# Kernel optimization log

Measured on AMD Instinct MI355X. Metric: run time of the kernel, lower is better.

## Reference

```python
import jax, jax.numpy as jnp
import numpy as np
import math

B, NOUT, NCLASSES, CENTER, TOPK = 1024, 512, 5994, 3, 5
M, SUB_M, SCALE = 0.2, -0.06, 30.0

COS_M, SIN_M = math.cos(M), math.sin(M)
TH, MM = math.cos(math.pi - M), math.sin(math.pi - M) * M
SUB_COS_M, SUB_SIN_M = math.cos(SUB_M), math.sin(SUB_M)
SUB_TH, SUB_MM = math.cos(math.pi - SUB_M), math.sin(math.pi - SUB_M) * SUB_M


def setup_inputs() -> dict:
    key = jax.random.key(0)
    k1, k2, k3 = jax.random.split(key, 3)
    x = jax.random.normal(k1, (B, NOUT), dtype=jnp.float32)
    # xavier_normal over (center, nClasses, nOut): fan_in=nClasses*nOut, fan_out=center*nOut
    std = math.sqrt(2.0 / (NCLASSES * NOUT + CENTER * NOUT))
    weight = jax.random.normal(k2, (CENTER, NCLASSES, NOUT), dtype=jnp.float32) * std
    label = jax.random.randint(k3, (B,), 0, NCLASSES, dtype=jnp.int64)
    return {"x": x, "weight": weight, "label": label}


def _l2norm(v, axis=-1, eps=1e-12):
    return v / jnp.maximum(jnp.linalg.norm(v, axis=axis, keepdims=True), eps)


def reference(x, weight, label):
    xn = _l2norm(x)                       # [B, j]
    wn = _l2norm(weight)                  # [a, c, j]
    cosine_subcen = jnp.einsum('bj,acj->bac', xn, wn)   # [B, center, C]
    cosine = jnp.max(cosine_subcen, axis=1)             # [B, C]

    sine = jnp.sqrt(jnp.clip(1.0 - cosine * cosine, 0.0, 1.0))
    phi = jnp.where(cosine - TH > 0, cosine * COS_M - sine * SIN_M, cosine - MM)
    sub_phi = jnp.where(cosine - SUB_TH > 0,
                        cosine * SUB_COS_M - sine * SUB_SIN_M,
                        cosine - SUB_MM)

    # topk+1 candidates; drop the label column if present, else drop the last
    _, idx = jax.lax.top_k(cosine, TOPK + 1)            # [B, topk+1]
    is_label = (idx == label[:, None].astype(idx.dtype))
    # stable sort pushes the (unique) label hit to the end, preserving order otherwise
    order = jnp.argsort(is_label.astype(jnp.int32), axis=1, stable=True)
    idx_fixed = jnp.take_along_axis(idx, order[:, :TOPK], axis=1)   # [B, topk]

    rows = jnp.arange(B)[:, None]
    one_hot_sub = jnp.zeros_like(cosine).at[rows, idx_fixed].add(1.0)
    one_hot = jax.nn.one_hot(label, NCLASSES, dtype=cosine.dtype)

    output = (one_hot * phi + one_hot_sub * sub_phi
              + (1.0 - one_hot_sub - one_hot) * cosine) * SCALE

    logp = jax.nn.log_softmax(output, axis=-1)
    loss = -jnp.mean(logp[jnp.arange(B), label])

    pred = jnp.argmax(cosine * SCALE, axis=-1)
    prec1 = jnp.mean((pred == label).astype(jnp.float32)) * 100.0
    return loss, prec1
```

## Files before the change

kernel.cpp:

```cpp
#include <hip/hip_runtime.h>
#include <math.h>

#define NB 1024
#define NC 5994
#define NCP 6144
#define NK 512
#define NA 3
#define NT 48
#define SCALE_F 30.0f
#define NPT 24

#define COS_M_F 0.9800665778412416f
#define SIN_M_F 0.19866933079506122f
#define TH_F (-0.9800665778412416f)
#define MM_F 0.039733866159012244f
#define SUB_COS_M_F 0.9982005399352042f
#define SUB_SIN_M_F (-0.05996400647944459f)
#define SUB_TH_F (-0.9982005399352042f)
#define SUB_MM_F 0.0035978403887666754f

typedef __attribute__((ext_vector_type(8))) short short8;
typedef __attribute__((ext_vector_type(4))) float f32x4;

__device__ __forceinline__ float waveReduceSum(float v) {
#pragma unroll
  for (int off = 32; off > 0; off >>= 1) v += __shfl_down(v, off);
  return v;
}

__device__ __forceinline__ void waveArgMax(float& v, int& i) {
#pragma unroll
  for (int off = 32; off > 0; off >>= 1) {
    float ov = __shfl_down(v, off);
    int oi = __shfl_down(i, off);
    if (ov > v || (ov == v && (unsigned)oi < (unsigned)i)) { v = ov; i = oi; }
  }
}

__device__ __forceinline__ ushort f2bf(float f) {
  unsigned u = __float_as_uint(f);
  u += 0x7FFFu + ((u >> 16) & 1u);
  return (ushort)(u >> 16);
}

__device__ __forceinline__ void load_lds16(const ushort* g, ushort* l) {
  __builtin_amdgcn_global_load_lds(
      (const __attribute__((address_space(1))) unsigned int*)g,
      (__attribute__((address_space(3))) unsigned int*)l, 16, 0, 0);
}

__global__ __launch_bounds__(256) void norm_convert(const float* __restrict__ x,
                                                    const float* __restrict__ w,
                                                    ushort* __restrict__ xb,
                                                    ushort* __restrict__ wb) {
  const int row = blockIdx.x * 4 + (threadIdx.x >> 6);
  const int lane = threadIdx.x & 63;
  const float* src;
  ushort* dst;
  if (row < NB) {
    src = x + (size_t)row * NK;
    dst = xb + (size_t)row * NK;
  } else {
    const int r = row - NB;
    const int a = r / NCP, c = r % NCP;
    dst = wb + (size_t)r * NK;
    if (c >= NC) {
      ushort4 z = {0, 0, 0, 0};
      *(ushort4*)(dst + lane * 4) = z;
      *(ushort4*)(dst + 256 + lane * 4) = z;
      return;
    }
    src = w + ((size_t)a * NC + c) * NK;
  }
  const float4 v0 = *(const float4*)(src + lane * 4);
  const float4 v1 = *(const float4*)(src + 256 + lane * 4);
  float ss = v0.x * v0.x + v0.y * v0.y + v0.z * v0.z + v0.w * v0.w +
             v1.x * v1.x + v1.y * v1.y + v1.z * v1.z + v1.w * v1.w;
  ss = waveReduceSum(ss);
  ss = __shfl(ss, 0);
  const float rn = 1.0f / fmaxf(sqrtf(ss), 1e-12f);
  ushort4 o0 = {f2bf(v0.x * rn), f2bf(v0.y * rn), f2bf(v0.z * rn), f2bf(v0.w * rn)};
  ushort4 o1 = {f2bf(v1.x * rn), f2bf(v1.y * rn), f2bf(v1.z * rn), f2bf(v1.w * rn)};
  *(ushort4*)(dst + lane * 4) = o0;
  *(ushort4*)(dst + 256 + lane * 4) = o1;
}

__global__ __launch_bounds__(128) void cos_gemm_mfma(const ushort* __restrict__ Xb,
                                                     const ushort* __restrict__ Wb,
                                                     float* __restrict__ cosine) {
  __shared__ ushort sA0[64 * 32];
  __shared__ ushort sA1[64 * 32];
  __shared__ ushort sB0[128 * 32];
  __shared__ ushort sB1[128 * 32];
  const int tid = threadIdx.x;
  const int lane = tid & 63;
  const int w = tid >> 6;

  const int id = blockIdx.x;
  const int cx = (id & 7) + ((id >> 7) << 3);
  const int by = (id >> 3) & 15;
  const int b0 = by * 64;
  const int c0 = cx * 128;

  const int lrow = lane >> 2;
  const int skg = ((lane & 3) - ((lane >> 3) & 3)) & 3;
  const ushort* gA = Xb + (size_t)(b0 + w * 32 + lrow) * NK + skg * 8;
  const ushort* gB = Wb + (size_t)(c0 + w * 64 + lrow) * NK + skg * 8;
  const int ldsA = w * 1024;
  const int ldsB = w * 2048;
  const int w4 = w * 4;

  const int r = lane & 15;
  const int kg = lane >> 4;
  const int rdoff = r * 32 + (((kg + (r >> 1)) & 3) * 8);

  f32x4 best[4][4];
  f32x4 acc[4][4];
#pragma unroll
  for (int i = 0; i < 4; ++i)
#pragma unroll
    for (int j = 0; j < 4; ++j) {
#pragma unroll
      for (int q = 0; q < 4; ++q) best[i][j][q] = -INFINITY;
      acc[i][j] = (f32x4)(0.f);
    }

  load_lds16(gA, (ushort*)sA0 + ldsA);
  load_lds16(gA + 16 * NK, (ushort*)sA0 + ldsA + 512);
#pragma unroll
  for (int j = 0; j < 4; ++j)
    load_lds16(gB + (size_t)j * 16 * NK, (ushort*)sB0 + ldsB + j * 512);
  __syncthreads();

#define GEMM_BODY(T, SAr, SBr, SAw, SBw)                                        \
  {                                                                             \
    const int t_ = (T);                                                         \
    if (t_ + 1 < NT) {                                                          \
      const int tn = t_ + 1;                                                    \
      const int k0 = (tn & 15) << 5;                                            \
      const size_t boff = (size_t)(tn >> 4) * NCP * NK + k0;                    \
      load_lds16(gA + k0, (ushort*)SAw + ldsA);                                 \
      load_lds16(gA + k0 + 16 * NK, (ushort*)SAw + ldsA + 512);                 \
      _Pragma("unroll") for (int j = 0; j < 4; ++j)                             \
          load_lds16(gB + boff + (size_t)j * 16 * NK,                           \
                     (ushort*)SBw + ldsB + j * 512);                            \
    }                                                                           \
    short8 af[4], bf[4];                                                        \
    _Pragma("unroll") for (int mi = 0; mi < 4; ++mi)                            \
        af[mi] = *(const short8*)&SAr[mi * 512 + rdoff];                        \
    _Pragma("unroll") for (int ni = 0; ni < 4; ++ni)                            \
        bf[ni] = *(const short8*)&SBr[(w4 + ni) * 512 + rdoff];                 \
    _Pragma("unroll") for (int mi = 0; mi < 4; ++mi)                            \
        _Pragma("unroll") for (int ni = 0; ni < 4; ++ni)                        \
            acc[mi][ni] = __builtin_amdgcn_mfma_f32_16x16x32_bf16(              \
                af[mi], bf[ni], acc[mi][ni], 0, 0, 0);                          \
    if ((t_ & 15) == 15) {                                                      \
      _Pragma("unroll") for (int i = 0; i < 4; ++i)                             \
          _Pragma("unroll") for (int j = 0; j < 4; ++j) {                       \
        _Pragma("unroll") for (int q = 0; q < 4; ++q)                           \
            best[i][j][q] = fmaxf(best[i][j][q], acc[i][j][q]);                 \
        acc[i][j] = (f32x4)(0.f);                                               \
      }                                                                         \
    }                                                                           \
    __syncthreads();                                                            \
  }

  for (int t = 0; t < NT; t += 2) {
    GEMM_BODY(t, sA0, sB0, sA1, sB1)
    GEMM_BODY(t + 1, sA1, sB1, sA0, sB0)
  }
#undef GEMM_BODY

  const int q4 = (lane >> 4) * 4;
#pragma unroll
  for (int ni = 0; ni < 4; ++ni) {
    const int col = c0 + w * 64 + ni * 16 + r;
    if (col < NC) {
#pragma unroll
      for (int mi = 0; mi < 4; ++mi) {
        const int row0 = b0 + mi * 16 + q4;
#pragma unroll
        for (int q = 0; q < 4; ++q)
          cosine[(size_t)(row0 + q) * NC + col] = best[mi][ni][q];
      }
    }
  }
}

__global__ __launch_bounds__(256) void row_loss(const float* __restrict__ cosine,
                                                const int* __restrict__ label,
                                                float* __restrict__ loss_b,
                                                float* __restrict__ corr_b) {
  __shared__ float swv[4];
  __shared__ int swi[4];
  __shared__ float s_red[4];
  __shared__ float s_maxv;
  __shared__ float s_cosL;
  __shared__ float topv[6];
  __shared__ int topi[6];

  const int b = blockIdx.x, tid = threadIdx.x;
  const int wv = tid >> 6;
  const int lab = label[b];
  const float* row = cosine + (size_t)b * NC;

  float v[NPT];
  float bv = -INFINITY;
  int bi = -1;
#pragma unroll
  for (int j = 0; j < NPT; ++j) {
    const int i = tid + j * 256;
    v[j] = (i < NC) ? row[i] : -INFINITY;
    if (v[j] > bv) { bv = v[j]; bi = i; }
  }
  if (tid == (lab & 255)) s_cosL = v[lab >> 8];
  waveArgMax(bv, bi);
  if ((tid & 63) == 0) { swv[wv] = bv; swi[wv] = bi; }
  __syncthreads();
  if (tid == 0) {
    float mv = swv[0]; int mi = swi[0];
    for (int q = 1; q < 4; ++q)
      if (swv[q] > mv || (swv[q] == mv && (unsigned)swi[q] < (unsigned)mi)) { mv = swv[q]; mi = swi[q]; }
    s_maxv = mv; topv[0] = mv; topi[0] = mi;
  }
  __syncthreads();
  const float maxv = s_maxv;

  float ps = 0.f;
#pragma unroll
  for (int j = 0; j < NPT; ++j) ps += __expf(SCALE_F * (v[j] - maxv));
  ps = waveReduceSum(ps);
  if ((tid & 63) == 0) s_red[wv] = ps;

  unsigned excl = 0;
  {
    const int wi = topi[0];
    if ((wi & 255) == tid) excl |= 1u << (wi >> 8);
  }

  for (int e = 1; e < 6; ++e) {
    float lv = -INFINITY;
    int li = -1;
#pragma unroll
    for (int j = 0; j < NPT; ++j)
      if (!((excl >> j) & 1u) && v[j] > lv) { lv = v[j]; li = tid + j * 256; }
    waveArgMax(lv, li);
    if ((tid & 63) == 0) { swv[wv] = lv; swi[wv] = li; }
    __syncthreads();
    if (tid == 0) {
      float mv = swv[0]; int mi = swi[0];
      for (int q = 1; q < 4; ++q)
        if (swv[q] > mv || (swv[q] == mv && (unsigned)swi[q] < (unsigned)mi)) { mv = swv[q]; mi = swi[q]; }
      topv[e] = mv; topi[e] = mi;
    }
    __syncthreads();
    const int wi = topi[e];
    if ((wi & 255) == tid) excl |= 1u << (wi >> 8);
  }

  if (tid == 0) {
    const float S = s_red[0] + s_red[1] + s_red[2] + s_red[3];
    const float m = SCALE_F * maxv;
    const float cosL = s_cosL;
    const float sineL = sqrtf(fminf(fmaxf(1.f - cosL * cosL, 0.f), 1.f));
    const float phiL = (cosL - TH_F > 0.f) ? (cosL * COS_M_F - sineL * SIN_M_F) : (cosL - MM_F);
    float adj = __expf(SCALE_F * phiL - m) - __expf(SCALE_F * cosL - m);
    int cnt = 0;
    for (int e = 0; e < 6 && cnt < 5; ++e) {
      if (topi[e] == lab) continue;
      const float c = topv[e];
      const float sine = sqrtf(fminf(fmaxf(1.f - c * c, 0.f), 1.f));
      const float sp = (c - SUB_TH_F > 0.f) ? (c * SUB_COS_M_F - sine * SUB_SIN_M_F) : (c - SUB_MM_F);
      adj += __expf(SCALE_F * sp - m) - __expf(SCALE_F * c - m);
      ++cnt;
    }
    const float Sp = S + adj;
    loss_b[b] = (logf(Sp) + m) - SCALE_F * phiL;
    corr_b[b] = (topi[0] == lab) ? 1.f : 0.f;
  }
}

__global__ __launch_bounds__(256) void finalize(const float* __restrict__ loss_b,
                                                const float* __restrict__ corr_b,
                                                float* __restrict__ out) {
  const int tid = threadIdx.x;
  float ls = 0.f, cs = 0.f;
  for (int i = tid; i < NB; i += 256) { ls += loss_b[i]; cs += corr_b[i]; }
  ls = waveReduceSum(ls);
  cs = waveReduceSum(cs);
  __shared__ float sl[4], sc[4];
  if ((tid & 63) == 0) { sl[tid >> 6] = ls; sc[tid >> 6] = cs; }
  __syncthreads();
  if (tid == 0) {
    const float L = sl[0] + sl[1] + sl[2] + sl[3];
    const float Cr = sc[0] + sc[1] + sc[2] + sc[3];
    out[0] = L / (float)NB;
    out[1] = Cr / (float)NB * 100.f;
  }
}

extern "C" void kernel_launch(void* const* d_in, const int* in_sizes, int n_in,
                              void* d_out, int out_size, void* d_ws, size_t ws_size,
                              hipStream_t stream) {
  const float* x = (const float*)d_in[0];
  const float* w = (const float*)d_in[1];
  const int* label = (const int*)d_in[2];
  float* out = (float*)d_out;
  char* ws = (char*)d_ws;

  ushort* xb = (ushort*)ws;
  ushort* wb = (ushort*)(ws + 1048576);
  float* cosine = (float*)(ws + 1048576 + 18874368);
  float* loss_b = (float*)ws;
  float* corr_b = (float*)(ws + 4096);

  norm_convert<<<(NB + NA * NCP) / 4, 256, 0, stream>>>(x, w, xb, wb);
  cos_gemm_mfma<<<16 * 48, 128, 0, stream>>>(xb, wb, cosine);
  row_loss<<<NB, 256, 0, stream>>>(cosine, label, loss_b, corr_b);
  finalize<<<1, 256, 0, stream>>>(loss_b, corr_b, out);
}
```

Measured before the change: 67.90 us.

## Deepen GEMM LDS pipeline to four buffers with prefetch distance two

The cosine GEMM goes from double-buffered LDS tiles to four rotating buffers, issuing global-to-LDS loads two k-steps ahead instead of one. Explicit s_waitcnt vmcnt counts wait only for the current tile's loads. A single raw s_barrier, fenced by sched_barriers, replaces the trailing __syncthreads. The aim is to hide more global-load latency behind the MFMA work and cut one barrier's stall per step. In exchange, LDS use per block doubles, which may lower occupancy, and correctness now depends on the hand-counted vmcnt values.

```diff
diff --git a/kernel.cpp b/kernel.cpp
--- a/kernel.cpp
+++ b/kernel.cpp
@@ -88,10 +88,8 @@
 __global__ __launch_bounds__(128) void cos_gemm_mfma(const ushort* __restrict__ Xb,
                                                      const ushort* __restrict__ Wb,
                                                      float* __restrict__ cosine) {
-  __shared__ ushort sA0[64 * 32];
-  __shared__ ushort sA1[64 * 32];
-  __shared__ ushort sB0[128 * 32];
-  __shared__ ushort sB1[128 * 32];
+  __shared__ ushort sA0[2048], sA1[2048], sA2[2048], sA3[2048];
+  __shared__ ushort sB0[4096], sB1[4096], sB2[4096], sB3[4096];
   const int tid = threadIdx.x;
   const int lane = tid & 63;
   const int w = tid >> 6;
@@ -125,26 +123,34 @@
       acc[i][j] = (f32x4)(0.f);
     }
 
-  load_lds16(gA, (ushort*)sA0 + ldsA);
-  load_lds16(gA + 16 * NK, (ushort*)sA0 + ldsA + 512);
-#pragma unroll
-  for (int j = 0; j < 4; ++j)
-    load_lds16(gB + (size_t)j * 16 * NK, (ushort*)sB0 + ldsB + j * 512);
-  __syncthreads();
+#define STAGE(TT, SAw, SBw)                                                     \
+  {                                                                             \
+    const int tt_ = (TT);                                                       \
+    const int k0 = (tt_ & 15) << 5;                                             \
+    const size_t boff = (size_t)(tt_ >> 4) * NCP * NK + k0;                     \
+    load_lds16(gA + k0, (ushort*)SAw + ldsA);                                   \
+    load_lds16(gA + k0 + 16 * NK, (ushort*)SAw + ldsA + 512);                   \
+    _Pragma("unroll") for (int j = 0; j < 4; ++j)                               \
+        load_lds16(gB + boff + (size_t)j * 16 * NK, (ushort*)SBw + ldsB + j * 512); \
+  }
+
+  STAGE(0, sA0, sB0)
+  STAGE(1, sA1, sB1)
 
 #define GEMM_BODY(T, SAr, SBr, SAw, SBw)                                        \
   {                                                                             \
     const int t_ = (T);                                                         \
-    if (t_ + 1 < NT) {                                                          \
-      const int tn = t_ + 1;                                                    \
-      const int k0 = (tn & 15) << 5;                                            \
-      const size_t boff = (size_t)(tn >> 4) * NCP * NK + k0;                    \
-      load_lds16(gA + k0, (ushort*)SAw + ldsA);                                 \
-      load_lds16(gA + k0 + 16 * NK, (ushort*)SAw + ldsA + 512);                 \
-      _Pragma("unroll") for (int j = 0; j < 4; ++j)                             \
-          load_lds16(gB + boff + (size_t)j * 16 * NK,                           \
-                     (ushort*)SBw + ldsB + j * 512);                            \
+    if (t_ + 2 < NT) STAGE(t_ + 2, SAw, SBw)                                    \
+    if (t_ + 2 < NT) {                                                          \
+      asm volatile("s_waitcnt vmcnt(12)" ::: "memory");    \
+    } else if (t_ + 1 < NT) {                                                   \
+      asm volatile("s_waitcnt vmcnt(6)" ::: "memory");                          \
+    } else {                                                                    \
+      asm volatile("s_waitcnt vmcnt(0)" ::: "memory");                          \
     }                                                                           \
+    __builtin_amdgcn_sched_barrier(0);                                          \
+    __builtin_amdgcn_s_barrier();                                               \
+    __builtin_amdgcn_sched_barrier(0);                                          \
     short8 af[4], bf[4];                                                        \
     _Pragma("unroll") for (int mi = 0; mi < 4; ++mi)                            \
         af[mi] = *(const short8*)&SAr[mi * 512 + rdoff];                        \
@@ -162,14 +168,16 @@
         acc[i][j] = (f32x4)(0.f);                                               \
       }                                                                         \
     }                                                                           \
-    __syncthreads();                                                            \
-  }
-
-  for (int t = 0; t < NT; t += 2) {
-    GEMM_BODY(t, sA0, sB0, sA1, sB1)
-    GEMM_BODY(t + 1, sA1, sB1, sA0, sB0)
+  }
+
+  for (int t = 0; t < NT; t += 4) {
+    GEMM_BODY(t,     sA0, sB0, sA2, sB2)
+    GEMM_BODY(t + 1, sA1, sB1, sA3, sB3)
+    GEMM_BODY(t + 2, sA2, sB2, sA0, sB0)
+    GEMM_BODY(t + 3, sA3, sB3, sA1, sB1)
   }
 #undef GEMM_BODY
+#undef STAGE
 
   const int q4 = (lane >> 4) * 4;
 #pragma unroll
```

After: 83.00 us. 22.2% more time.
